# Kernel tuning notes

Measured on AMD Instinct MI355X. Metric: run time of the kernel, lower is better.

The kernel has to match this reference:

```python
import jax, jax.numpy as jnp
import numpy as np

K = 128           # top-k
NUM_SAMPLES = 500 # perturbation samples
SIGMA = 0.05      # noise scale (forward arg sigma in the torch module)


def setup_inputs() -> dict:
    key = jax.random.key(0)
    k1, k2 = jax.random.split(key)
    x = jax.random.normal(k1, (32, 2048), dtype=jnp.float32)
    noise = jax.random.normal(k2, (32, NUM_SAMPLES, 2048), dtype=jnp.float32)
    return {"x": x, "noise": noise}


def reference(x, noise):
    # x: (b, d) scores; noise: (b, n, d) standard-normal perturbations.
    b, d = x.shape
    n = noise.shape[1]
    perturbed = x[:, None, :] + noise * SIGMA          # (b, n, d)
    _, idx = jax.lax.top_k(perturbed, K)               # (b, n, K) indices into d
    idx = jnp.sort(idx, axis=-1)                       # sorted, matching torch.sort
    # indicators[b,j,d] = mean_n one_hot(idx[b,n,j], d)
    # Computed with a scatter-add instead of materializing the (b,n,K,d) one-hot.
    bi = jnp.arange(b)[:, None, None]                  # (b,1,1)
    ki = jnp.arange(K)[None, None, :]                  # (1,1,K)
    counts = jnp.zeros((b, K, d), dtype=x.dtype).at[bi, ki, idx].add(1.0)
    indicators = counts / n                            # (b, K, d)
    return indicators, idx
```

## Files before the change

### kernel.cpp

```cpp
#include <hip/hip_runtime.h>


constexpr int B_     = 32;
constexpr int D_     = 2048;
constexpr int NS_    = 500;
constexpr int TOPK_  = 128;
constexpr int SLACK_ = 32;
constexpr float SIGMA_  = 0.05f;
constexpr int PER_LANE_ = D_ / 64;
constexpr int WAVES_PER_BLOCK_ = 4;
constexpr int CAP_   = 256;
constexpr int SLOTS_ = CAP_ / 64;
constexpr int JCHUNK_ = 8;

__device__ __forceinline__ uint32_t order_key(float f) {
  uint32_t u = __float_as_uint(f);
  return (u & 0x80000000u) ? ~u : (u | 0x80000000u);
}
__device__ __forceinline__ float inv_key(uint32_t k) {
  uint32_t u = (k & 0x80000000u) ? (k & 0x7FFFFFFFu) : ~k;
  return __uint_as_float(u);
}

__global__ __launch_bounds__(64) void ptk_cutoff(const float* __restrict__ x,
                                                 float* __restrict__ cutf) {
  const int lane = threadIdx.x & 63;
  const int b = blockIdx.x;
  const float* __restrict__ xr = x + (size_t)b * D_;
  uint32_t keys[PER_LANE_];
#pragma unroll
  for (int j = 0; j < PER_LANE_; j += 4) {
    const float4 xv = *reinterpret_cast<const float4*>(xr + lane * PER_LANE_ + j);
    keys[j + 0] = order_key(xv.x); keys[j + 1] = order_key(xv.y);
    keys[j + 2] = order_key(xv.z); keys[j + 3] = order_key(xv.w);
  }
  uint32_t prefix = 0; int k = TOPK_ + SLACK_;
#pragma unroll 1
  for (int bit = 31; bit >= 0; --bit) {
    const uint32_t want = (prefix >> bit) | 1u;
    int c = 0;
#pragma unroll
    for (int j = 0; j < PER_LANE_; ++j) c += ((keys[j] >> bit) == want) ? 1 : 0;
#pragma unroll
    for (int off = 32; off >= 1; off >>= 1) c += __shfl_xor(c, off);
    if (c >= k) prefix |= (1u << bit); else k -= c;
  }
  if (lane == 0) cutf[b] = inv_key(prefix);
}

__global__ __launch_bounds__(256) void ptk_select(
    const float* __restrict__ x, const float* __restrict__ noise,
    const float* __restrict__ cutf, float* __restrict__ out_idx) {
  __shared__ uint2 comp[WAVES_PER_BLOCK_][CAP_];

  const int lane = threadIdx.x & 63;
  const int wave = threadIdx.x >> 6;
  const int row  = blockIdx.x * WAVES_PER_BLOCK_ + wave;
  const int b = row / NS_;

  const float* __restrict__ xr = x + (size_t)b * D_;
  const float* __restrict__ nr = noise + (size_t)row * D_;
  const int base_i = lane * PER_LANE_;

  float p[PER_LANE_];
#pragma unroll
  for (int j = 0; j < PER_LANE_; j += 4) {
    const float4 nv = *reinterpret_cast<const float4*>(nr + base_i + j);
    const float4 xv = *reinterpret_cast<const float4*>(xr + base_i + j);
    p[j + 0] = fmaf(SIGMA_, nv.x, xv.x);
    p[j + 1] = fmaf(SIGMA_, nv.y, xv.y);
    p[j + 2] = fmaf(SIGMA_, nv.z, xv.z);
    p[j + 3] = fmaf(SIGMA_, nv.w, xv.w);
  }

  const float cf = cutf[b];

  uint32_t m = 0;
#pragma unroll
  for (int j = 0; j < PER_LANE_; ++j) m |= (p[j] >= cf) ? (1u << j) : 0u;
  const int cnt = __popc(m);

  const uint64_t below = (lane == 0) ? 0ull : ((~0ull) >> (64 - lane));
  int offset = 0, C = 0;
#pragma unroll
  for (int t = 0; t < 6; ++t) {
    const uint64_t mb = __ballot((cnt >> t) & 1);
    offset += (int)__popcll(mb & below) << t;
    C      += (int)__popcll(mb) << t;
  }

  float* __restrict__ idx_row = out_idx + (size_t)row * TOPK_;

  if (C >= TOPK_ && C <= CAP_) {
    {
      uint32_t mm = m; int q = offset;
      while (mm) {
        const int j = __ffs(mm) - 1; mm &= mm - 1;
        comp[wave][q] = make_uint2(order_key(p[j]), (uint32_t)(base_i + j));
        ++q;
      }
    }
    __asm__ volatile("s_waitcnt lgkmcnt(0)" ::: "memory");

    uint32_t kk[SLOTS_], ki[SLOTS_];
    bool valid[SLOTS_];
#pragma unroll
    for (int s = 0; s < SLOTS_; ++s) {
      const int q = (s << 6) + lane;
      valid[s] = (q < C);
      const uint2 v = valid[s] ? comp[wave][q] : make_uint2(0u, 0u);
      kk[s] = v.x; ki[s] = v.y;
    }

    uint32_t orv = 0u, andv = 0xFFFFFFFFu;
#pragma unroll
    for (int s = 0; s < SLOTS_; ++s) {
      orv  |= valid[s] ? kk[s] : 0u;
      andv &= valid[s] ? kk[s] : 0xFFFFFFFFu;
    }
#pragma unroll
    for (int off = 32; off >= 1; off >>= 1) {
      orv  |= __shfl_xor(orv, off);
      andv &= __shfl_xor(andv, off);
    }
    const uint32_t diff = orv ^ andv;

    uint32_t prefix; int r;
    if (diff == 0u) {
      prefix = orv; r = TOPK_;
    } else {
      const int startbit = 31 - __clz(diff);
      prefix = (startbit == 31) ? 0u : (andv & (0xFFFFFFFFu << (startbit + 1)));
      int k = TOPK_;
      int A = C;
#pragma unroll 1
      for (int bit = startbit; bit >= 0; --bit) {
        const uint32_t want = (prefix >> bit) | 1u;
        int c = 0;
#pragma unroll
        for (int s = 0; s < SLOTS_; ++s)
          c += __popcll(__ballot((kk[s] >> bit) == want));
        if (c >= k) { prefix |= (1u << bit); A = c; }
        else        { k -= c; A -= c; }
        if (A == 1) {
          uint32_t mykey = 0u; bool have = false;
#pragma unroll
          for (int s = 0; s < SLOTS_; ++s) {
            const bool hit = valid[s] && ((kk[s] >> bit) == (prefix >> bit));
            mykey = hit ? kk[s] : mykey;
            have |= hit;
          }
          const uint64_t mb = __ballot(have);
          const int src = __ffsll((unsigned long long)mb) - 1;
          prefix = __shfl(mykey, src);
          k = 1;
          break;
        }
      }
      r = k;
    }

    int sel_run = 0, eq_run = 0;
#pragma unroll
    for (int s = 0; s < SLOTS_; ++s) {
      const bool gt = kk[s] > prefix;
      const bool eq = kk[s] == prefix;
      const uint64_t meq = __ballot(eq);
      const int eqrank = eq_run + __popcll(meq & below);
      const bool sel = gt || (eq && (eqrank < r));
      const uint64_t msel = __ballot(sel);
      if (sel) {
        const int pos = sel_run + __popcll(msel & below);
        idx_row[pos] = (float)(int)ki[s];
      }
      sel_run += __popcll(msel);
      eq_run  += __popcll(meq);
    }
  } else {
    uint32_t keys[PER_LANE_];
#pragma unroll
    for (int j = 0; j < PER_LANE_; ++j) keys[j] = order_key(p[j]);

    uint32_t prefix = 0; int k = TOPK_;
#pragma unroll 1
    for (int bit = 31; bit >= 0; --bit) {
      const uint32_t want = (prefix >> bit) | 1u;
      int c = 0;
#pragma unroll
      for (int j = 0; j < PER_LANE_; ++j) c += ((keys[j] >> bit) == want) ? 1 : 0;
#pragma unroll
      for (int off = 32; off >= 1; off >>= 1) c += __shfl_xor(c, off);
      if (c >= k) prefix |= (1u << bit); else k -= c;
    }
    const int r = k;

    int gt = 0, eq = 0;
#pragma unroll
    for (int j = 0; j < PER_LANE_; ++j) {
      gt += (keys[j] > prefix) ? 1 : 0;
      eq += (keys[j] == prefix) ? 1 : 0;
    }
    uint32_t incl2 = (uint32_t)gt | ((uint32_t)eq << 16);
#pragma unroll
    for (int off = 1; off < 64; off <<= 1) {
      uint32_t y = __shfl_up(incl2, (unsigned)off);
      if (lane >= off) incl2 += y;
    }
    const int gt_base = (int)(incl2 & 0xFFFFu) - gt;
    const int eq_base = (int)(incl2 >> 16) - eq;
    int pos = gt_base + min(eq_base, r);
    int eq_seen = eq_base;
#pragma unroll
    for (int j = 0; j < PER_LANE_; ++j) {
      const uint32_t kj = keys[j];
      bool s = false;
      if (kj > prefix) s = true;
      else if (kj == prefix) { s = (eq_seen < r); eq_seen++; }
      if (s) { idx_row[pos] = (float)(base_i + j); pos++; }
    }
  }
}

__global__ __launch_bounds__(256) void ptk_hist(
    const float* __restrict__ out_idx, float* __restrict__ indicators) {
  __shared__ int hist[JCHUNK_][D_];

  const int tid   = threadIdx.x;
  const int b     = blockIdx.x >> 4;
  const int chunk = blockIdx.x & 15;
  const int j0    = chunk * JCHUNK_;

  int4* h4 = (int4*)hist;
  for (int t = tid; t < JCHUNK_ * D_ / 4; t += 256)
    h4[t] = make_int4(0, 0, 0, 0);
  __syncthreads();

  const float* __restrict__ src = out_idx + (size_t)b * NS_ * TOPK_ + j0;
  for (int t = tid; t < NS_ * 2; t += 256) {
    const int n = t >> 1;
    const int q = (t & 1) << 2;
    const float4 v = *reinterpret_cast<const float4*>(src + (size_t)n * TOPK_ + q);
    atomicAdd(&hist[q + 0][(int)v.x], 1);
    atomicAdd(&hist[q + 1][(int)v.y], 1);
    atomicAdd(&hist[q + 2][(int)v.z], 1);
    atomicAdd(&hist[q + 3][(int)v.w], 1);
  }
  __syncthreads();

  float4* __restrict__ dst =
      (float4*)(indicators + ((size_t)b * TOPK_ + j0) * D_);
  for (int t = tid; t < JCHUNK_ * D_ / 4; t += 256) {
    const int4 h = h4[t];
    float4 o;
    o.x = (float)h.x / (float)NS_;
    o.y = (float)h.y / (float)NS_;
    o.z = (float)h.z / (float)NS_;
    o.w = (float)h.w / (float)NS_;
    dst[t] = o;
  }
}

extern "C" void kernel_launch(void* const* d_in, const int* in_sizes, int n_in,
                              void* d_out, int out_size, void* d_ws, size_t ws_size,
                              hipStream_t stream) {
  const float* x     = (const float*)d_in[0];
  const float* noise = (const float*)d_in[1];
  float* indicators  = (float*)d_out;
  float* out_idx     = (float*)d_out + (size_t)B_ * TOPK_ * D_;
  float* cutf        = (float*)d_ws;

  hipLaunchKernelGGL(ptk_cutoff, dim3(B_), dim3(64), 0, stream, x, cutf);

  const int rows = B_ * NS_;
  hipLaunchKernelGGL(ptk_select, dim3(rows / WAVES_PER_BLOCK_), dim3(256), 0,
                     stream, x, noise, cutf, out_idx);

  hipLaunchKernelGGL(ptk_hist, dim3(B_ * 16), dim3(256), 0, stream,
                     out_idx, indicators);
}
```

Before: 232.3 us.

## Split each select row across two waves that share compaction via LDS

```diff
diff --git a/kernel.cpp b/kernel.cpp
--- a/kernel.cpp
+++ b/kernel.cpp
@@ -8,7 +8,8 @@
 constexpr int SLACK_ = 32;
 constexpr float SIGMA_  = 0.05f;
 constexpr int PER_LANE_ = D_ / 64;
-constexpr int WAVES_PER_BLOCK_ = 4;
+constexpr int HALF_  = D_ / 2;
+constexpr int HPL_   = HALF_ / 64;
 constexpr int CAP_   = 256;
 constexpr int SLOTS_ = CAP_ / 64;
 constexpr int JCHUNK_ = 8;
@@ -51,22 +52,26 @@
 __global__ __launch_bounds__(256) void ptk_select(
     const float* __restrict__ x, const float* __restrict__ noise,
     const float* __restrict__ cutf, float* __restrict__ out_idx) {
-  __shared__ uint2 comp[WAVES_PER_BLOCK_][CAP_];
+  __shared__ uint2 comp[2][2 * CAP_];
+  __shared__ int cnts[2][2];
 
   const int lane = threadIdx.x & 63;
   const int wave = threadIdx.x >> 6;
-  const int row  = blockIdx.x * WAVES_PER_BLOCK_ + wave;
+  const int pair = wave >> 1;
+  const int half = wave & 1;
+  const int row  = blockIdx.x * 2 + pair;
   const int b = row / NS_;
 
-  const float* __restrict__ xr = x + (size_t)b * D_;
-  const float* __restrict__ nr = noise + (size_t)row * D_;
-  const int base_i = lane * PER_LANE_;
-
-  float p[PER_LANE_];
-#pragma unroll
-  for (int j = 0; j < PER_LANE_; j += 4) {
-    const float4 nv = *reinterpret_cast<const float4*>(nr + base_i + j);
-    const float4 xv = *reinterpret_cast<const float4*>(xr + base_i + j);
+  const float* __restrict__ xr = x + (size_t)b * D_ + half * HALF_;
+  const float* __restrict__ nr = noise + (size_t)row * D_ + half * HALF_;
+  const int base_l = lane * HPL_;
+  const int base_i = half * HALF_ + base_l;
+
+  float p[HPL_];
+#pragma unroll
+  for (int j = 0; j < HPL_; j += 4) {
+    const float4 nv = *reinterpret_cast<const float4*>(nr + base_l + j);
+    const float4 xv = *reinterpret_cast<const float4*>(xr + base_l + j);
     p[j + 0] = fmaf(SIGMA_, nv.x, xv.x);
     p[j + 1] = fmaf(SIGMA_, nv.y, xv.y);
     p[j + 2] = fmaf(SIGMA_, nv.z, xv.z);
@@ -77,38 +82,46 @@
 
   uint32_t m = 0;
 #pragma unroll
-  for (int j = 0; j < PER_LANE_; ++j) m |= (p[j] >= cf) ? (1u << j) : 0u;
+  for (int j = 0; j < HPL_; ++j) m |= (p[j] >= cf) ? (1u << j) : 0u;
   const int cnt = __popc(m);
 
   const uint64_t below = (lane == 0) ? 0ull : ((~0ull) >> (64 - lane));
-  int offset = 0, C = 0;
-#pragma unroll
-  for (int t = 0; t < 6; ++t) {
+  int offset = 0, Cw = 0;
+#pragma unroll
+  for (int t = 0; t < 5; ++t) {
     const uint64_t mb = __ballot((cnt >> t) & 1);
     offset += (int)__popcll(mb & below) << t;
-    C      += (int)__popcll(mb) << t;
-  }
+    Cw     += (int)__popcll(mb) << t;
+  }
+  if (lane == 0) cnts[pair][half] = Cw;
+
+  {
+    uint32_t mm = m; int q = half * CAP_ + offset;
+    while (mm) {
+      const int j = __ffs(mm) - 1; mm &= mm - 1;
+      comp[pair][q] = make_uint2(order_key(p[j]), (uint32_t)(base_i + j));
+      ++q;
+    }
+  }
+  __syncthreads();
+
+  if (half) return;
+
+  const int C0 = cnts[pair][0];
+  const int C1 = cnts[pair][1];
+  const int C  = C0 + C1;
 
   float* __restrict__ idx_row = out_idx + (size_t)row * TOPK_;
 
   if (C >= TOPK_ && C <= CAP_) {
-    {
-      uint32_t mm = m; int q = offset;
-      while (mm) {
-        const int j = __ffs(mm) - 1; mm &= mm - 1;
-        comp[wave][q] = make_uint2(order_key(p[j]), (uint32_t)(base_i + j));
-        ++q;
-      }
-    }
-    __asm__ volatile("s_waitcnt lgkmcnt(0)" ::: "memory");
-
     uint32_t kk[SLOTS_], ki[SLOTS_];
     bool valid[SLOTS_];
 #pragma unroll
     for (int s = 0; s < SLOTS_; ++s) {
       const int q = (s << 6) + lane;
+      const int a = (q < C0) ? q : (CAP_ + q - C0);
       valid[s] = (q < C);
-      const uint2 v = valid[s] ? comp[wave][q] : make_uint2(0u, 0u);
+      const uint2 v = valid[s] ? comp[pair][a] : make_uint2(0u, 0u);
       kk[s] = v.x; ki[s] = v.y;
     }
 
@@ -177,9 +190,13 @@
       eq_run  += __popcll(meq);
     }
   } else {
+    const float* __restrict__ xr2 = x + (size_t)b * D_;
+    const float* __restrict__ nr2 = noise + (size_t)row * D_;
+    const int bi = lane * PER_LANE_;
     uint32_t keys[PER_LANE_];
 #pragma unroll
-    for (int j = 0; j < PER_LANE_; ++j) keys[j] = order_key(p[j]);
+    for (int j = 0; j < PER_LANE_; ++j)
+      keys[j] = order_key(fmaf(SIGMA_, nr2[bi + j], xr2[bi + j]));
 
     uint32_t prefix = 0; int k = TOPK_;
 #pragma unroll 1
@@ -216,7 +233,7 @@
       bool s = false;
       if (kj > prefix) s = true;
       else if (kj == prefix) { s = (eq_seen < r); eq_seen++; }
-      if (s) { idx_row[pos] = (float)(base_i + j); pos++; }
+      if (s) { idx_row[pos] = (float)(bi + j); pos++; }
     }
   }
 }
@@ -272,8 +289,8 @@
   hipLaunchKernelGGL(ptk_cutoff, dim3(B_), dim3(64), 0, stream, x, cutf);
 
   const int rows = B_ * NS_;
-  hipLaunchKernelGGL(ptk_select, dim3(rows / WAVES_PER_BLOCK_), dim3(256), 0,
-                     stream, x, noise, cutf, out_idx);
+  hipLaunchKernelGGL(ptk_select, dim3(rows / 2), dim3(256), 0, stream,
+                     x, noise, cutf, out_idx);
 
   hipLaunchKernelGGL(ptk_hist, dim3(B_ * 16), dim3(256), 0, stream,
                      out_idx, indicators);
```

Measured after the change: 224.1 us. 3.5% less time.
